# Optimization experiments

Hardware: AMD Instinct MI355X
Metric: run time of the kernel (lower is better)

The kernel has to match this reference:

```python
import jax, jax.numpy as jnp
import numpy as np

B, N, C = 8, 2048, 256
NGRP = 4          # n oscillator dims per group
RANK = 16         # A_rank
EPS = 1e-6        # solver eps
GN_EPS = 1e-5     # torch GroupNorm default eps


def setup_inputs() -> dict:
    key = jax.random.key(0)
    k0, k1, k2, k3 = jax.random.split(key, 4)
    x = jax.random.normal(k0, (B, N, C), jnp.float32)
    y = jax.random.normal(k1, (B, C, N), jnp.float32)
    sc = jax.random.uniform(k2, (B, N, N), jnp.float32)
    U = 0.01 * jax.random.normal(k3, (N, RANK), jnp.float32)
    omega_param = (1.0 / np.sqrt(2)).astype(np.float32) * jnp.ones((C // 2, 1), jnp.float32)
    gn_w = jnp.ones((C,), jnp.float32)
    gn_b = jnp.zeros((C,), jnp.float32)
    gamma = jnp.float32(1.0)
    return {"x": x, "y": y, "sc": sc, "U": U, "omega_param": omega_param,
            "gn_w": gn_w, "gn_b": gn_b, "gamma": gamma, "Q": 8}


def _map_to_sphere(x):
    # normalize each group of NGRP channels to unit norm
    xv = x.reshape(B, N, C // NGRP, NGRP)
    n2 = jnp.clip(jnp.sum(xv * xv, axis=-1, keepdims=True), EPS, None)
    return (xv * jax.lax.rsqrt(n2)).reshape(B, N, C)


def _project_osc(v, x):
    # remove component of v along x within each oscillator group (tangent projection)
    xv = x.reshape(B, N, C // NGRP, NGRP)
    vv = v.reshape(B, N, C // NGRP, NGRP)
    sim = jnp.sum(xv * vv, axis=-1, keepdims=True)
    return (vv - sim * xv).reshape(B, N, C)


def _group_norm(y, w, b):
    # y: [B, C, N]; num_groups = C // NGRP, NGRP channels per group
    G = C // NGRP
    yv = y.reshape(B, G, NGRP * N)
    mu = jnp.mean(yv, axis=-1, keepdims=True)
    var = jnp.mean((yv - mu) ** 2, axis=-1, keepdims=True)
    yn = ((yv - mu) * jax.lax.rsqrt(var + GN_EPS)).reshape(B, C, N)
    return yn * w[None, :, None] + b[None, :, None]


def _omega_term(x, omega_param):
    # pairwise rotation: (x0, x1) -> (omg*x1, -omg*x0), omg = |omega_param| per pair
    xp = x.reshape(B, N, C // 2, 2)
    omg = jnp.abs(omega_param).reshape(1, 1, C // 2)  # norm over trailing dim of size 1
    out = jnp.stack([omg * xp[..., 1], -omg * xp[..., 0]], axis=-1)
    return out.reshape(B, N, C)


def _kuramoto(x, y, sc, U, omega_param, gn_w, gn_b, gamma, Q):
    rho = 1.0
    # y: [B, C, N] -> GroupNorm -> [B, N, C] -> sphere
    y = _group_norm(y, gn_w, gn_b)
    y = _map_to_sphere(jnp.transpose(y, (0, 2, 1)))
    # x: [B, N, C] (N != C so no transpose in original)
    x = _map_to_sphere(x)
    # coupling matrix K = sym(W) * sigmoid(U U^T)  (normalize_K=False, w_scale=1)
    Wsym = 0.5 * (sc + jnp.transpose(sc, (0, 2, 1)))
    A = jax.nn.sigmoid(U @ U.T)          # [N, N]
    K = Wsym * A[None, :, :]             # [B, N, N]

    def step(xc, _):
        coupling = jnp.einsum('bnm,bmc->bnc', K, xc)
        force = coupling + y
        om = _omega_term(xc, omega_param)
        dxdt = om + rho * _project_osc(force, xc)
        xn = _map_to_sphere(xc + gamma * dxdt)
        return xn, xn

    _, xs = jax.lax.scan(step, x, None, length=Q)
    return xs  # [Q, B, N, C]


def reference(x, y, sc, U, omega_param, gn_w, gn_b, gamma, Q):
    return _kuramoto(x, y, sc, U, omega_param, gn_w, gn_b, gamma, Q)
```

## Files before the change

### kernel.cpp

```cpp
#include <hip/hip_runtime.h>
#include <hip/hip_bf16.h>

#define BB 8
#define NN 2048
#define CC 256
#define GG 64
#define QQ 8

typedef unsigned short u16;
typedef __attribute__((ext_vector_type(8))) short bf16x8;
typedef __attribute__((ext_vector_type(4))) float f32x4;

static __device__ __forceinline__ float b2f(u16 u) {
  union { unsigned int i; float f; } cv; cv.i = ((unsigned int)u) << 16; return cv.f;
}
static __device__ __forceinline__ u16 f2b(float f) {
  union { __hip_bfloat16 h; u16 u; } cv; cv.h = __float2bfloat16(f); return cv.u;
}
static __device__ __forceinline__ float ldin(const void* p, size_t i, bool f32) {
  return f32 ? ((const float*)p)[i] : b2f(((const u16*)p)[i]);
}
static __device__ __forceinline__ float4 ldin4(const void* p, size_t i, bool f32) {
  if (f32) return *(const float4*)((const float*)p + i);
  ushort4 u = *(const ushort4*)((const u16*)p + i);
  return make_float4(b2f(u.x), b2f(u.y), b2f(u.z), b2f(u.w));
}
static __device__ __forceinline__ void gload16(const void* g, void* l) {
  __builtin_amdgcn_global_load_lds(
      (const __attribute__((address_space(1))) void*)g,
      (__attribute__((address_space(3))) void*)l, 16, 0, 0);
}

__global__ __launch_bounds__(256) void detect_kernel(const u16* __restrict__ sc,
                                                     int* __restrict__ flag)
{
  __shared__ int sh;
  if (threadIdx.x == 0) sh = 0;
  __syncthreads();
  int cnt = 0;
  for (int i = threadIdx.x; i < 2048; i += 256) {
    u16 w = sc[2 * i];
    int e = (w >> 7) & 0xFF;
    if (e >= 100 && e <= 130) cnt++;
  }
  atomicAdd(&sh, cnt);
  __syncthreads();
  if (threadIdx.x == 0) *flag = (sh < 1024) ? 1 : 0;
}

__global__ __launch_bounds__(256) void build_k_kernel(
    const void* __restrict__ sc, const void* __restrict__ U,
    u16* __restrict__ Khi, u16* __restrict__ Klo,
    const int* __restrict__ flagp, int b0, int nbat)
{
  const int i0 = blockIdx.y * 32;
  const int j0 = blockIdx.x * 32;
  if (j0 < i0) return;
  const bool f32 = (*flagp != 0);
  const int tx = threadIdx.x;
  const int ty = threadIdx.y;
  const int t  = ty * 32 + tx;
  const int rr = t >> 3;
  const int cq = t & 7;

  __shared__ float Ui[32][17];
  __shared__ float Uj[32][17];
  __shared__ float As[32][33];
  __shared__ float t1[32][33];
  __shared__ float t2[32][33];

  for (int s = t; s < 512; s += 256) {
    int r2 = s >> 4, kk = s & 15;
    Ui[r2][kk] = ldin(U, (size_t)(i0 + r2) * 16 + kk, f32);
    Uj[r2][kk] = ldin(U, (size_t)(j0 + r2) * 16 + kk, f32);
  }
  __syncthreads();
  for (int ii = ty; ii < 32; ii += 8) {
    float dot = 0.f;
    #pragma unroll
    for (int k = 0; k < 16; k++) dot += Ui[ii][k] * Uj[tx][k];
    As[ii][tx] = 1.0f / (1.0f + expf(-dot));
  }

  for (int bl = 0; bl < nbat; bl++) {
    const int b = b0 + bl;
    const size_t scb = (size_t)b * NN * NN;
    __syncthreads();
    float4 va = ldin4(sc, scb + (size_t)(i0 + rr) * NN + j0 + 4 * cq, f32);
    float4 vb = ldin4(sc, scb + (size_t)(j0 + rr) * NN + i0 + 4 * cq, f32);
    t1[rr][4*cq+0] = va.x; t1[rr][4*cq+1] = va.y;
    t1[rr][4*cq+2] = va.z; t1[rr][4*cq+3] = va.w;
    t2[rr][4*cq+0] = vb.x; t2[rr][4*cq+1] = vb.y;
    t2[rr][4*cq+2] = vb.z; t2[rr][4*cq+3] = vb.w;
    __syncthreads();
    const size_t kfb = (size_t)bl * NN * NN;
    ushort4 h4, l4;
    #pragma unroll
    for (int k = 0; k < 4; k++) {
      int col = 4 * cq + k;
      float kv = 0.5f * (t1[rr][col] + t2[col][rr]) * As[rr][col];
      u16 h = f2b(kv);
      ((u16*)&h4)[k] = h;
      ((u16*)&l4)[k] = f2b(kv - b2f(h));
    }
    size_t o = kfb + (size_t)(i0 + rr) * NN + j0 + 4 * cq;
    *(ushort4*)(Khi + o) = h4;
    *(ushort4*)(Klo + o) = l4;
    if (i0 != j0) {
      #pragma unroll
      for (int k = 0; k < 4; k++) {
        int col = 4 * cq + k;
        float kv = 0.5f * (t2[rr][col] + t1[col][rr]) * As[col][rr];
        u16 h = f2b(kv);
        ((u16*)&h4)[k] = h;
        ((u16*)&l4)[k] = f2b(kv - b2f(h));
      }
      size_t o2 = kfb + (size_t)(j0 + rr) * NN + i0 + 4 * cq;
      *(ushort4*)(Khi + o2) = h4;
      *(ushort4*)(Klo + o2) = l4;
    }
  }
}

__global__ __launch_bounds__(256) void gn_stats_kernel(
    const void* __restrict__ y, float* __restrict__ murs,
    const int* __restrict__ flagp)
{
  const bool f32 = (*flagp != 0);
  const int bg = blockIdx.x;
  float s = 0.f, ss = 0.f;
  if (f32) {
    const float* base = (const float*)y + (size_t)bg * 4 * NN;
    for (int i = threadIdx.x; i < 2048; i += 256) {
      float4 v = *(const float4*)(base + (size_t)i * 4);
      s  += v.x + v.y + v.z + v.w;
      ss += v.x*v.x + v.y*v.y + v.z*v.z + v.w*v.w;
    }
  } else {
    const u16* base = (const u16*)y + (size_t)bg * 4 * NN;
    for (int i = threadIdx.x; i < 2048; i += 256) {
      ushort4 v = *(const ushort4*)(base + (size_t)i * 4);
      float f0 = b2f(v.x), f1 = b2f(v.y), f2 = b2f(v.z), f3 = b2f(v.w);
      s  += f0 + f1 + f2 + f3;
      ss += f0*f0 + f1*f1 + f2*f2 + f3*f3;
    }
  }
  #pragma unroll
  for (int off = 32; off > 0; off >>= 1) {
    s  += __shfl_down(s, off, 64);
    ss += __shfl_down(ss, off, 64);
  }
  __shared__ float sh[8];
  const int w = threadIdx.x >> 6, ln = threadIdx.x & 63;
  if (ln == 0) { sh[w * 2] = s; sh[w * 2 + 1] = ss; }
  __syncthreads();
  if (threadIdx.x == 0) {
    float S  = sh[0] + sh[2] + sh[4] + sh[6];
    float SS = sh[1] + sh[3] + sh[5] + sh[7];
    float mu  = S / 8192.0f;
    float var = SS / 8192.0f - mu * mu;
    murs[bg * 2]     = mu;
    murs[bg * 2 + 1] = 1.0f / sqrtf(fmaxf(var, 0.f) + 1e-5f);
  }
}

__global__ __launch_bounds__(256) void y_tf_kernel(
    const void* __restrict__ y, const float* __restrict__ murs,
    const void* __restrict__ gw, const void* __restrict__ gb,
    float* __restrict__ yt, const int* __restrict__ flagp)
{
  const bool f32 = (*flagp != 0);
  const int b = blockIdx.y;
  const int n = blockIdx.x * 64 + threadIdx.x;
  for (int g = threadIdx.y; g < GG; g += 4) {
    float mu = murs[(b * GG + g) * 2];
    float rs = murs[(b * GG + g) * 2 + 1];
    float v[4];
    #pragma unroll
    for (int k = 0; k < 4; k++) {
      int c = 4 * g + k;
      float val = (ldin(y, ((size_t)b * CC + c) * NN + n, f32) - mu) * rs;
      v[k] = val * ldin(gw, c, f32) + ldin(gb, c, f32);
    }
    float n2 = v[0]*v[0] + v[1]*v[1] + v[2]*v[2] + v[3]*v[3];
    float scl = 1.0f / sqrtf(fmaxf(n2, 1e-6f));
    float4 o; o.x = v[0]*scl; o.y = v[1]*scl; o.z = v[2]*scl; o.w = v[3]*scl;
    *(float4*)(yt + ((size_t)b * NN + n) * CC + 4 * g) = o;
  }
}

__global__ __launch_bounds__(256) void x_init_kernel(
    const void* __restrict__ x, u16* __restrict__ xTh, u16* __restrict__ xTl,
    const int* __restrict__ flagp)
{
  const bool f32 = (*flagp != 0);
  const int b = blockIdx.y;
  const int n = blockIdx.x * 64 + threadIdx.x;
  for (int g = threadIdx.y; g < GG; g += 4) {
    size_t idx = ((size_t)b * NN + n) * CC + 4 * g;
    float v[4];
    if (f32) {
      float4 u4 = *(const float4*)((const float*)x + idx);
      v[0] = u4.x; v[1] = u4.y; v[2] = u4.z; v[3] = u4.w;
    } else {
      ushort4 u = *(const ushort4*)((const u16*)x + idx);
      v[0] = b2f(u.x); v[1] = b2f(u.y); v[2] = b2f(u.z); v[3] = b2f(u.w);
    }
    float n2 = v[0]*v[0] + v[1]*v[1] + v[2]*v[2] + v[3]*v[3];
    float scl = 1.0f / sqrtf(fmaxf(n2, 1e-6f));
    size_t xb = ((size_t)b * CC + 4 * g) * NN + n;
    #pragma unroll
    for (int k = 0; k < 4; k++) {
      float xv = v[k] * scl;
      u16 h = f2b(xv);
      xTh[xb + (size_t)k * NN] = h;
      xTl[xb + (size_t)k * NN] = f2b(xv - b2f(h));
    }
  }
}

static __device__ __forceinline__ void fused_step_epilogue(
    f32x4 (&acc)[2][2], int b, int m0, int c0, int wr, int wc, int l15, int lk,
    const u16* __restrict__ xhc, const u16* __restrict__ xlc,
    u16* __restrict__ xhn, u16* __restrict__ xln,
    const float* __restrict__ yt, const void* __restrict__ omega,
    const void* __restrict__ gamma, void* __restrict__ outbase, size_t qoff,
    bool f32)
{
  const float gm = ldin(gamma, 0, f32);
  #pragma unroll
  for (int fr = 0; fr < 2; fr++) {
    const int rbase = m0 + wr * 32 + fr * 16 + lk * 4;
    #pragma unroll
    for (int fc = 0; fc < 2; fc++) {
      const int c = c0 + wc * 32 + fc * 16 + l15;
      const size_t xoff = ((size_t)b * CC + c) * NN + rbase;
      ushort4 xh4 = *(const ushort4*)(xhc + xoff);
      ushort4 xl4 = *(const ushort4*)(xlc + xoff);
      float xcv[4] = { b2f(xh4.x) + b2f(xl4.x), b2f(xh4.y) + b2f(xl4.y),
                       b2f(xh4.z) + b2f(xl4.z), b2f(xh4.w) + b2f(xl4.w) };
      float om   = fabsf(ldin(omega, c >> 1, f32));
      float omsg = (c & 1) ? -om : om;
      float xn[4];
      #pragma unroll
      for (int r = 0; r < 4; r++) {
        const int n = rbase + r;
        float f = acc[fr][fc][r] + yt[((size_t)b * NN + n) * CC + c];
        float s = xcv[r] * f;
        s += __shfl_xor(s, 1);
        s += __shfl_xor(s, 2);
        float xp = __shfl_xor(xcv[r], 1);
        float d  = omsg * xp + (f - s * xcv[r]);
        float v  = xcv[r] + gm * d;
        float n2 = v * v;
        n2 += __shfl_xor(n2, 1);
        n2 += __shfl_xor(n2, 2);
        float scl = 1.0f / sqrtf(fmaxf(n2, 1e-6f));
        xn[r] = v * scl;
        const size_t oidx = qoff + ((size_t)b * NN + n) * CC + c;
        if (f32) ((float*)outbase)[oidx] = xn[r];
        else     ((u16*)outbase)[oidx]   = f2b(xn[r]);
      }
      ushort4 nh, nl;
      #pragma unroll
      for (int r = 0; r < 4; r++) {
        u16 h = f2b(xn[r]);
        ((u16*)&nh)[r] = h;
        ((u16*)&nl)[r] = f2b(xn[r] - b2f(h));
      }
      *(ushort4*)(xhn + xoff) = nh;
      *(ushort4*)(xln + xoff) = nl;
    }
  }
}

__global__ __launch_bounds__(256, 4) void gemm_fused_sb(
    const u16* __restrict__ Khi, const u16* __restrict__ Klo,
    const u16* __restrict__ xhc, const u16* __restrict__ xlc,
    u16* __restrict__ xhn, u16* __restrict__ xln,
    const float* __restrict__ yt, const void* __restrict__ omega,
    const void* __restrict__ gamma, void* __restrict__ outbase, size_t qoff,
    const int* __restrict__ flagp)
{
  const int flat = blockIdx.x + 4 * blockIdx.y + 128 * blockIdx.z;
  const int swz  = (flat & 7) * 128 + (flat >> 3);
  const int bx = swz & 3;
  const int by = (swz >> 2) & 31;
  const int b  = swz >> 7;
  const int m0 = by * 64;
  const int c0 = bx * 64;

  __shared__ char lds[32768];

  const int t    = threadIdx.x;
  const int lane = t & 63;
  const int wid  = t >> 6;
  const int wr   = wid >> 1;
  const int wc   = wid & 1;

  const u16* Ah = Khi + (size_t)b * NN * NN;
  const u16* Al = Klo + (size_t)b * NN * NN;
  const u16* Bh = xhc + (size_t)b * CC * NN;
  const u16* Bl = xlc + (size_t)b * CC * NN;

  const int tr   = t >> 3;
  const int phys = (t & 7) ^ (tr & 7);
  const size_t aoff = (size_t)(m0 + tr) * NN + phys * 8;
  const size_t boff = (size_t)(c0 + tr) * NN + phys * 8;
  const int dst = wid * 1024;

  f32x4 acc[2][2];
  const f32x4 zero4 = {0.f, 0.f, 0.f, 0.f};
  #pragma unroll
  for (int i = 0; i < 2; i++)
    #pragma unroll
    for (int j = 0; j < 2; j++) acc[i][j] = zero4;

  const int l15 = lane & 15;
  const int lk  = lane >> 4;

  for (int kt = 0; kt < NN / 64; kt++) {
    const int k0 = kt * 64;
    #pragma unroll
    for (int i = 0; i < 2; i++) {
      gload16(Ah + aoff + (size_t)i * (32 * NN) + k0, lds +         i * 4096 + dst);
      gload16(Al + aoff + (size_t)i * (32 * NN) + k0, lds +  8192 + i * 4096 + dst);
      gload16(Bh + boff + (size_t)i * (32 * NN) + k0, lds + 16384 + i * 4096 + dst);
      gload16(Bl + boff + (size_t)i * (32 * NN) + k0, lds + 24576 + i * 4096 + dst);
    }
    __syncthreads();
    #pragma unroll
    for (int ks = 0; ks < 2; ks++) {
      const int cl = ks * 4 + lk;
      bf16x8 fah[2], fal[2], fbh[2], fbl[2];
      #pragma unroll
      for (int fr = 0; fr < 2; fr++) {
        int r   = wr * 32 + fr * 16 + l15;
        int off = r * 128 + ((cl ^ (r & 7)) << 4);
        fah[fr] = *(const bf16x8*)(lds + off);
        fal[fr] = *(const bf16x8*)(lds + 8192 + off);
      }
      #pragma unroll
      for (int fc = 0; fc < 2; fc++) {
        int r   = wc * 32 + fc * 16 + l15;
        int off = r * 128 + ((cl ^ (r & 7)) << 4);
        fbh[fc] = *(const bf16x8*)(lds + 16384 + off);
        fbl[fc] = *(const bf16x8*)(lds + 24576 + off);
      }
      #pragma unroll
      for (int fr = 0; fr < 2; fr++)
        #pragma unroll
        for (int fc = 0; fc < 2; fc++) {
          acc[fr][fc] = __builtin_amdgcn_mfma_f32_16x16x32_bf16(
              fah[fr], fbh[fc], acc[fr][fc], 0, 0, 0);
          acc[fr][fc] = __builtin_amdgcn_mfma_f32_16x16x32_bf16(
              fah[fr], fbl[fc], acc[fr][fc], 0, 0, 0);
          acc[fr][fc] = __builtin_amdgcn_mfma_f32_16x16x32_bf16(
              fal[fr], fbh[fc], acc[fr][fc], 0, 0, 0);
        }
    }
    __syncthreads();
  }

  fused_step_epilogue(acc, b, m0, c0, wr, wc, l15, lk,
                      xhc, xlc, xhn, xln, yt, omega, gamma,
                      outbase, qoff, (*flagp != 0));
}

__global__ __launch_bounds__(256, 2) void gemm_fused_db(
    const u16* __restrict__ Khi, const u16* __restrict__ Klo,
    const u16* __restrict__ xhc, const u16* __restrict__ xlc,
    u16* __restrict__ xhn, u16* __restrict__ xln,
    const float* __restrict__ yt, const void* __restrict__ omega,
    const void* __restrict__ gamma, void* __restrict__ outbase, size_t qoff,
    const int* __restrict__ flagp, int grp)
{
  const int flat = blockIdx.x + 4 * blockIdx.y + 128 * blockIdx.z;
  const int swz  = (flat & 7) * 64 + (flat >> 3);
  const int bx = swz & 3;
  const int by = (swz >> 2) & 31;
  const int bl = swz >> 7;
  const int b  = grp * 4 + bl;
  const int m0 = by * 64;
  const int c0 = bx * 64;

  __shared__ char lds[2][32768];

  const int t    = threadIdx.x;
  const int lane = t & 63;
  const int wid  = t >> 6;
  const int wr   = wid >> 1;
  const int wc   = wid & 1;

  const u16* Ah = Khi + (size_t)bl * NN * NN;
  const u16* Al = Klo + (size_t)bl * NN * NN;
  const u16* Bh = xhc + (size_t)b * CC * NN;
  const u16* Bl = xlc + (size_t)b * CC * NN;

  const int tr   = t >> 3;
  const int phys = (t & 7) ^ (tr & 7);
  const size_t aoff = (size_t)(m0 + tr) * NN + phys * 8;
  const size_t boff = (size_t)(c0 + tr) * NN + phys * 8;
  const int dst = wid * 1024;

  f32x4 acc[2][2];
  const f32x4 zero4 = {0.f, 0.f, 0.f, 0.f};
  #pragma unroll
  for (int i = 0; i < 2; i++)
    #pragma unroll
    for (int j = 0; j < 2; j++) acc[i][j] = zero4;

  auto stage = [&](int bufi, int kt) {
    char* base = &lds[bufi][0];
    const int k0 = kt * 64;
    #pragma unroll
    for (int i = 0; i < 2; i++) {
      gload16(Ah + aoff + (size_t)i * (32 * NN) + k0, base +         i * 4096 + dst);
      gload16(Al + aoff + (size_t)i * (32 * NN) + k0, base +  8192 + i * 4096 + dst);
      gload16(Bh + boff + (size_t)i * (32 * NN) + k0, base + 16384 + i * 4096 + dst);
      gload16(Bl + boff + (size_t)i * (32 * NN) + k0, base + 24576 + i * 4096 + dst);
    }
  };

  const int l15 = lane & 15;
  const int lk  = lane >> 4;

  auto compute = [&](int bufi) {
    const char* base = &lds[bufi][0];
    #pragma unroll
    for (int ks = 0; ks < 2; ks++) {
      const int cl = ks * 4 + lk;
      bf16x8 fah[2], fal[2], fbh[2], fbl[2];
      #pragma unroll
      for (int fr = 0; fr < 2; fr++) {
        int r   = wr * 32 + fr * 16 + l15;
        int off = r * 128 + ((cl ^ (r & 7)) << 4);
        fah[fr] = *(const bf16x8*)(base + off);
        fal[fr] = *(const bf16x8*)(base + 8192 + off);
      }
      #pragma unroll
      for (int fc = 0; fc < 2; fc++) {
        int r   = wc * 32 + fc * 16 + l15;
        int off = r * 128 + ((cl ^ (r & 7)) << 4);
        fbh[fc] = *(const bf16x8*)(base + 16384 + off);
        fbl[fc] = *(const bf16x8*)(base + 24576 + off);
      }
      #pragma unroll
      for (int fr = 0; fr < 2; fr++)
        #pragma unroll
        for (int fc = 0; fc < 2; fc++) {
          acc[fr][fc] = __builtin_amdgcn_mfma_f32_16x16x32_bf16(
              fah[fr], fbh[fc], acc[fr][fc], 0, 0, 0);
          acc[fr][fc] = __builtin_amdgcn_mfma_f32_16x16x32_bf16(
              fah[fr], fbl[fc], acc[fr][fc], 0, 0, 0);
          acc[fr][fc] = __builtin_amdgcn_mfma_f32_16x16x32_bf16(
              fal[fr], fbh[fc], acc[fr][fc], 0, 0, 0);
        }
    }
  };

  stage(0, 0);
  __syncthreads();
  int buf = 0;
  for (int kt = 0; kt < NN / 64; kt++) {
    if (kt + 1 < NN / 64) stage(buf ^ 1, kt + 1);
    compute(buf);
    __syncthreads();
    buf ^= 1;
  }

  fused_step_epilogue(acc, b, m0, c0, wr, wc, l15, lk,
                      xhc, xlc, xhn, xln, yt, omega, gamma,
                      outbase, qoff, (*flagp != 0));
}

extern "C" void kernel_launch(void* const* d_in, const int* in_sizes, int n_in,
                              void* d_out, int out_size, void* d_ws, size_t ws_size,
                              hipStream_t stream) {
  const void* x     = d_in[0];
  const void* y     = d_in[1];
  const void* sc    = d_in[2];
  const void* U     = d_in[3];
  const void* omega = d_in[4];
  const void* gw    = d_in[5];
  const void* gb    = d_in[6];
  const void* gamma = d_in[7];
  char* ws = (char*)d_ws;

  const size_t BNC = (size_t)BB * NN * CC;
  const bool big = ws_size >= 184600000ull;

  if (big) {
    u16*   Khi  = (u16*)(ws);
    u16*   Klo  = (u16*)(ws + 67108864);
    float* yt   = (float*)(ws + 134217728);
    u16*   xAh  = (u16*)(ws + 150994944);
    u16*   xAl  = (u16*)(ws + 159383552);
    u16*   xBh  = (u16*)(ws + 167772160);
    u16*   xBl  = (u16*)(ws + 176160768);
    float* murs = (float*)(ws + 184549376);
    int*   flag = (int*)  (ws + 184553472);
    u16* xh[2] = { xAh, xBh };
    u16* xl[2] = { xAl, xBl };

    detect_kernel<<<dim3(1), dim3(256), 0, stream>>>((const u16*)sc, flag);
    gn_stats_kernel<<<dim3(512), dim3(256), 0, stream>>>(y, murs, flag);
    y_tf_kernel<<<dim3(32, 8), dim3(64, 4), 0, stream>>>(y, murs, gw, gb, yt, flag);
    x_init_kernel<<<dim3(32, 8), dim3(64, 4), 0, stream>>>(x, xAh, xAl, flag);
    build_k_kernel<<<dim3(64, 64), dim3(32, 8), 0, stream>>>(
        sc, U, Khi, Klo, flag, 0, 8);
    for (int q = 0; q < QQ; q++) {
      const int cur = q & 1, nxt = cur ^ 1;
      gemm_fused_sb<<<dim3(4, 32, 8), dim3(256), 0, stream>>>(
          Khi, Klo, xh[cur], xl[cur], xh[nxt], xl[nxt],
          yt, omega, gamma, d_out, (size_t)q * BNC, flag);
    }
  } else {
    u16*   Khi  = (u16*)(ws);
    u16*   Klo  = (u16*)(ws + 33554432);
    float* yt   = (float*)(ws + 67108864);
    u16*   xAh  = (u16*)(ws + 83886080);
    u16*   xAl  = (u16*)(ws + 92274688);
    u16*   xBh  = (u16*)(ws + 100663296);
    u16*   xBl  = (u16*)(ws + 109051904);
    float* murs = (float*)(ws + 117440512);
    int*   flag = (int*)  (ws + 117444608);
    u16* xh[2] = { xAh, xBh };
    u16* xl[2] = { xAl, xBl };

    detect_kernel<<<dim3(1), dim3(256), 0, stream>>>((const u16*)sc, flag);
    gn_stats_kernel<<<dim3(512), dim3(256), 0, stream>>>(y, murs, flag);
    y_tf_kernel<<<dim3(32, 8), dim3(64, 4), 0, stream>>>(y, murs, gw, gb, yt, flag);
    x_init_kernel<<<dim3(32, 8), dim3(64, 4), 0, stream>>>(x, xAh, xAl, flag);
    for (int grp = 0; grp < 2; grp++) {
      build_k_kernel<<<dim3(64, 64), dim3(32, 8), 0, stream>>>(
          sc, U, Khi, Klo, flag, grp * 4, 4);
      for (int q = 0; q < QQ; q++) {
        const int cur = q & 1, nxt = cur ^ 1;
        gemm_fused_db<<<dim3(4, 32, 4), dim3(256), 0, stream>>>(
            Khi, Klo, xh[cur], xl[cur], xh[nxt], xl[nxt],
            yt, omega, gamma, d_out, (size_t)q * BNC, flag, grp);
      }
    }
  }
}
```

Baseline: 927.0 us.

## Use 128x128 tiles with 8 waves and double-buffered LDS pipeline in step GEMM

Replaces the single-buffered 64x64, 4-wave step GEMM with a 128x128-tile kernel of 512 threads (8 waves). It uses two 64 KB LDS buffers and explicit vmcnt waits so global loads for tile k+2 overlap compute on tile k. The larger tiles raise reuse of the K and x fragments and cut global traffic, and the pipelining hides load latency. In exchange the grid shrinks to 256 blocks, which may underfill the CUs, and the 128 KB of LDS per block limits occupancy to one block per CU.

```diff
diff --git a/kernel.cpp b/kernel.cpp
--- a/kernel.cpp
+++ b/kernel.cpp
@@ -219,8 +219,9 @@
   }
 }
 
+template<int NFR, int NFC>
 static __device__ __forceinline__ void fused_step_epilogue(
-    f32x4 (&acc)[2][2], int b, int m0, int c0, int wr, int wc, int l15, int lk,
+    f32x4 (&acc)[NFR][NFC], int b, int rb, int cb, int l15, int lk,
     const u16* __restrict__ xhc, const u16* __restrict__ xlc,
     u16* __restrict__ xhn, u16* __restrict__ xln,
     const float* __restrict__ yt, const void* __restrict__ omega,
@@ -229,11 +230,11 @@
 {
   const float gm = ldin(gamma, 0, f32);
   #pragma unroll
-  for (int fr = 0; fr < 2; fr++) {
-    const int rbase = m0 + wr * 32 + fr * 16 + lk * 4;
-    #pragma unroll
-    for (int fc = 0; fc < 2; fc++) {
-      const int c = c0 + wc * 32 + fc * 16 + l15;
+  for (int fr = 0; fr < NFR; fr++) {
+    const int rbase = rb + fr * 16 + lk * 4;
+    #pragma unroll
+    for (int fc = 0; fc < NFC; fc++) {
+      const int c = cb + fc * 16 + l15;
       const size_t xoff = ((size_t)b * CC + c) * NN + rbase;
       ushort4 xh4 = *(const ushort4*)(xhc + xoff);
       ushort4 xl4 = *(const ushort4*)(xlc + xoff);
@@ -274,7 +275,7 @@
   }
 }
 
-__global__ __launch_bounds__(256, 4) void gemm_fused_sb(
+__global__ __launch_bounds__(512, 2) void gemm_fused_sk(
     const u16* __restrict__ Khi, const u16* __restrict__ Klo,
     const u16* __restrict__ xhc, const u16* __restrict__ xlc,
     u16* __restrict__ xhn, u16* __restrict__ xln,
@@ -282,15 +283,134 @@
     const void* __restrict__ gamma, void* __restrict__ outbase, size_t qoff,
     const int* __restrict__ flagp)
 {
+  const int flat = blockIdx.x + 2 * blockIdx.y + 32 * blockIdx.z;
+  const int swz  = (flat & 7) * 32 + (flat >> 3);
+  const int bx = swz & 1;
+  const int by = (swz >> 1) & 15;
+  const int b  = swz >> 5;
+  const int m0 = by * 128;
+  const int c0 = bx * 128;
+
+  __shared__ char lds[2][65536];
+
+  const int t    = threadIdx.x;
+  const int lane = t & 63;
+  const int wid  = t >> 6;
+  const int ng   = wid >> 2;
+  const int wr   = (wid >> 1) & 1;
+  const int wc   = wid & 1;
+
+  const u16* Ah = Khi + (size_t)b * NN * NN;
+  const u16* Al = Klo + (size_t)b * NN * NN;
+  const u16* Bh = xhc + (size_t)b * CC * NN;
+  const u16* Bl = xlc + (size_t)b * CC * NN;
+
+  const int tr   = t >> 3;
+  const int phys = (t & 7) ^ (tr & 7);
+  const size_t aoff = (size_t)(m0 + tr) * NN + phys * 8;
+  const size_t boff = (size_t)(c0 + tr) * NN + phys * 8;
+  const int dst = wid * 1024;
+
+  f32x4 acc[4][2];
+  const f32x4 zero4 = {0.f, 0.f, 0.f, 0.f};
+  #pragma unroll
+  for (int i = 0; i < 4; i++)
+    #pragma unroll
+    for (int j = 0; j < 2; j++) acc[i][j] = zero4;
+
+  auto stage = [&](int bufi, int kt) {
+    char* base = &lds[bufi][0];
+    const int k0 = kt * 64;
+    #pragma unroll
+    for (int i = 0; i < 2; i++) {
+      gload16(Ah + aoff + (size_t)i * (64 * NN) + k0, base +         i * 8192 + dst);
+      gload16(Al + aoff + (size_t)i * (64 * NN) + k0, base + 16384 + i * 8192 + dst);
+      gload16(Bh + boff + (size_t)i * (64 * NN) + k0, base + 32768 + i * 8192 + dst);
+      gload16(Bl + boff + (size_t)i * (64 * NN) + k0, base + 49152 + i * 8192 + dst);
+    }
+  };
+
+  const int l15 = lane & 15;
+  const int lk  = lane >> 4;
+
+  auto compute = [&](int bufi) {
+    const char* base = &lds[bufi][0];
+    #pragma unroll
+    for (int ks = 0; ks < 2; ks++) {
+      const int cl = ks * 4 + lk;
+      bf16x8 fah[4], fal[4], fbh[2], fbl[2];
+      #pragma unroll
+      for (int fr = 0; fr < 4; fr++) {
+        int r   = wr * 64 + fr * 16 + l15;
+        int off = r * 128 + ((cl ^ (r & 7)) << 4);
+        fah[fr] = *(const bf16x8*)(base + off);
+        fal[fr] = *(const bf16x8*)(base + 16384 + off);
+      }
+      #pragma unroll
+      for (int fc = 0; fc < 2; fc++) {
+        int r   = ng * 64 + wc * 32 + fc * 16 + l15;
+        int off = r * 128 + ((cl ^ (r & 7)) << 4);
+        fbh[fc] = *(const bf16x8*)(base + 32768 + off);
+        fbl[fc] = *(const bf16x8*)(base + 49152 + off);
+      }
+      #pragma unroll
+      for (int fr = 0; fr < 4; fr++)
+        #pragma unroll
+        for (int fc = 0; fc < 2; fc++) {
+          acc[fr][fc] = __builtin_amdgcn_mfma_f32_16x16x32_bf16(
+              fah[fr], fbh[fc], acc[fr][fc], 0, 0, 0);
+          acc[fr][fc] = __builtin_amdgcn_mfma_f32_16x16x32_bf16(
+              fah[fr], fbl[fc], acc[fr][fc], 0, 0, 0);
+          acc[fr][fc] = __builtin_amdgcn_mfma_f32_16x16x32_bf16(
+              fal[fr], fbh[fc], acc[fr][fc], 0, 0, 0);
+        }
+    }
+  };
+
+  stage(0, 0);
+  stage(1, 1);
+  for (int kt = 0; kt < 30; kt++) {
+    asm volatile("s_waitcnt vmcnt(8)" ::: "memory");
+    __builtin_amdgcn_s_barrier();
+    __builtin_amdgcn_sched_barrier(0);
+    compute(kt & 1);
+    asm volatile("s_waitcnt lgkmcnt(0)" ::: "memory");
+    __builtin_amdgcn_sched_barrier(0);
+    __builtin_amdgcn_s_barrier();
+    stage(kt & 1, kt + 2);
+  }
+  asm volatile("s_waitcnt vmcnt(8)" ::: "memory");
+  __builtin_amdgcn_s_barrier();
+  __builtin_amdgcn_sched_barrier(0);
+  compute(0);
+  asm volatile("s_waitcnt vmcnt(0)" ::: "memory");
+  __builtin_amdgcn_s_barrier();
+  __builtin_amdgcn_sched_barrier(0);
+  compute(1);
+
+  fused_step_epilogue<4, 2>(acc, b, m0 + wr * 64, c0 + ng * 64 + wc * 32,
+                            l15, lk, xhc, xlc, xhn, xln, yt, omega, gamma,
+                            outbase, qoff, (*flagp != 0));
+}
+
+__global__ __launch_bounds__(256, 2) void gemm_fused_db(
+    const u16* __restrict__ Khi, const u16* __restrict__ Klo,
+    const u16* __restrict__ xhc, const u16* __restrict__ xlc,
+    u16* __restrict__ xhn, u16* __restrict__ xln,
+    const float* __restrict__ yt, const void* __restrict__ omega,
+    const void* __restrict__ gamma, void* __restrict__ outbase, size_t qoff,
+    const int* __restrict__ flagp, int grp)
+{
   const int flat = blockIdx.x + 4 * blockIdx.y + 128 * blockIdx.z;
-  const int swz  = (flat & 7) * 128 + (flat >> 3);
+  const int swz  = (flat & 7) * 64 + (flat >> 3);
   const int bx = swz & 3;
   const int by = (swz >> 2) & 31;
-  const int b  = swz >> 7;
+  const int bl = swz >> 7;
+  const int b  = grp * 4 + bl;
   const int m0 = by * 64;
   const int c0 = bx * 64;
 
-  __shared__ char lds[32768];
+  __shared__ char lds[2][32768];
 
   const int t    = threadIdx.x;
   const int lane = t & 63;
@@ -298,8 +418,8 @@
   const int wr   = wid >> 1;
   const int wc   = wid & 1;
 
-  const u16* Ah = Khi + (size_t)b * NN * NN;
-  const u16* Al = Klo + (size_t)b * NN * NN;
+  const u16* Ah = Khi + (size_t)bl * NN * NN;
+  const u16* Al = Klo + (size_t)bl * NN * NN;
   const u16* Bh = xhc + (size_t)b * CC * NN;
   const u16* Bl = xlc + (size_t)b * CC * NN;
 
@@ -316,19 +436,23 @@
     #pragma unroll
     for (int j = 0; j < 2; j++) acc[i][j] = zero4;
 
+  auto stage = [&](int bufi, int kt) {
+    char* base = &lds[bufi][0];
+    const int k0 = kt * 64;
+    #pragma unroll
+    for (int i = 0; i < 2; i++) {
+      gload16(Ah + aoff + (size_t)i * (32 * NN) + k0, base +         i * 4096 + dst);
+      gload16(Al + aoff + (size_t)i * (32 * NN) + k0, base +  8192 + i * 4096 + dst);
+      gload16(Bh + boff + (size_t)i * (32 * NN) + k0, base + 16384 + i * 4096 + dst);
+      gload16(Bl + boff + (size_t)i * (32 * NN) + k0, base + 24576 + i * 4096 + dst);
+    }
+  };
+
   const int l15 = lane & 15;
   const int lk  = lane >> 4;
 
-  for (int kt = 0; kt < NN / 64; kt++) {
-    const int k0 = kt * 64;
-    #pragma unroll
-    for (int i = 0; i < 2; i++) {
-      gload16(Ah + aoff + (size_t)i * (32 * NN) + k0, lds +         i * 4096 + dst);
-      gload16(Al + aoff + (size_t)i * (32 * NN) + k0, lds +  8192 + i * 4096 + dst);
-      gload16(Bh + boff + (size_t)i * (32 * NN) + k0, lds + 16384 + i * 4096 + dst);
-      gload16(Bl + boff + (size_t)i * (32 * NN) + k0, lds + 24576 + i * 4096 + dst);
-    }
-    __syncthreads();
+  auto compute = [&](int bufi) {
+    const char* base = &lds[bufi][0];
     #pragma unroll
     for (int ks = 0; ks < 2; ks++) {
       const int cl = ks * 4 + lk;
@@ -337,15 +461,15 @@
       for (int fr = 0; fr < 2; fr++) {
         int r   = wr * 32 + fr * 16 + l15;
         int off = r * 128 + ((cl ^ (r & 7)) << 4);
-        fah[fr] = *(const bf16x8*)(lds + off);
-        fal[fr] = *(const bf16x8*)(lds + 8192 + off);
+        fah[fr] = *(const bf16x8*)(base + off);
+        fal[fr] = *(const bf16x8*)(base + 8192 + off);
       }
       #pragma unroll
       for (int fc = 0; fc < 2; fc++) {
         int r   = wc * 32 + fc * 16 + l15;
         int off = r * 128 + ((cl ^ (r & 7)) << 4);
-        fbh[fc] = *(const bf16x8*)(lds + 16384 + off);
-        fbl[fc] = *(const bf16x8*)(lds + 24576 + off);
+        fbh[fc] = *(const bf16x8*)(base + 16384 + off);
+        fbl[fc] = *(const bf16x8*)(base + 24576 + off);
       }
       #pragma unroll
       for (int fr = 0; fr < 2; fr++)
@@ -359,104 +483,6 @@
               fal[fr], fbh[fc], acc[fr][fc], 0, 0, 0);
         }
     }
-    __syncthreads();
-  }
-
-  fused_step_epilogue(acc, b, m0, c0, wr, wc, l15, lk,
-                      xhc, xlc, xhn, xln, yt, omega, gamma,
-                      outbase, qoff, (*flagp != 0));
-}
-
-__global__ __launch_bounds__(256, 2) void gemm_fused_db(
-    const u16* __restrict__ Khi, const u16* __restrict__ Klo,
-    const u16* __restrict__ xhc, const u16* __restrict__ xlc,
-    u16* __restrict__ xhn, u16* __restrict__ xln,
-    const float* __restrict__ yt, const void* __restrict__ omega,
-    const void* __restrict__ gamma, void* __restrict__ outbase, size_t qoff,
-    const int* __restrict__ flagp, int grp)
-{
-  const int flat = blockIdx.x + 4 * blockIdx.y + 128 * blockIdx.z;
-  const int swz  = (flat & 7) * 64 + (flat >> 3);
-  const int bx = swz & 3;
-  const int by = (swz >> 2) & 31;
-  const int bl = swz >> 7;
-  const int b  = grp * 4 + bl;
-  const int m0 = by * 64;
-  const int c0 = bx * 64;
-
-  __shared__ char lds[2][32768];
-
-  const int t    = threadIdx.x;
-  const int lane = t & 63;
-  const int wid  = t >> 6;
-  const int wr   = wid >> 1;
-  const int wc   = wid & 1;
-
-  const u16* Ah = Khi + (size_t)bl * NN * NN;
-  const u16* Al = Klo + (size_t)bl * NN * NN;
-  const u16* Bh = xhc + (size_t)b * CC * NN;
-  const u16* Bl = xlc + (size_t)b * CC * NN;
-
-  const int tr   = t >> 3;
-  const int phys = (t & 7) ^ (tr & 7);
-  const size_t aoff = (size_t)(m0 + tr) * NN + phys * 8;
-  const size_t boff = (size_t)(c0 + tr) * NN + phys * 8;
-  const int dst = wid * 1024;
-
-  f32x4 acc[2][2];
-  const f32x4 zero4 = {0.f, 0.f, 0.f, 0.f};
-  #pragma unroll
-  for (int i = 0; i < 2; i++)
-    #pragma unroll
-    for (int j = 0; j < 2; j++) acc[i][j] = zero4;
-
-  auto stage = [&](int bufi, int kt) {
-    char* base = &lds[bufi][0];
-    const int k0 = kt * 64;
-    #pragma unroll
-    for (int i = 0; i < 2; i++) {
-      gload16(Ah + aoff + (size_t)i * (32 * NN) + k0, base +         i * 4096 + dst);
-      gload16(Al + aoff + (size_t)i * (32 * NN) + k0, base +  8192 + i * 4096 + dst);
-      gload16(Bh + boff + (size_t)i * (32 * NN) + k0, base + 16384 + i * 4096 + dst);
-      gload16(Bl + boff + (size_t)i * (32 * NN) + k0, base + 24576 + i * 4096 + dst);
-    }
-  };
-
-  const int l15 = lane & 15;
-  const int lk  = lane >> 4;
-
-  auto compute = [&](int bufi) {
-    const char* base = &lds[bufi][0];
-    #pragma unroll
-    for (int ks = 0; ks < 2; ks++) {
-      const int cl = ks * 4 + lk;
-      bf16x8 fah[2], fal[2], fbh[2], fbl[2];
-      #pragma unroll
-      for (int fr = 0; fr < 2; fr++) {
-        int r   = wr * 32 + fr * 16 + l15;
-        int off = r * 128 + ((cl ^ (r & 7)) << 4);
-        fah[fr] = *(const bf16x8*)(base + off);
-        fal[fr] = *(const bf16x8*)(base + 8192 + off);
-      }
-      #pragma unroll
-      for (int fc = 0; fc < 2; fc++) {
-        int r   = wc * 32 + fc * 16 + l15;
-        int off = r * 128 + ((cl ^ (r & 7)) << 4);
-        fbh[fc] = *(const bf16x8*)(base + 16384 + off);
-        fbl[fc] = *(const bf16x8*)(base + 24576 + off);
-      }
-      #pragma unroll
-      for (int fr = 0; fr < 2; fr++)
-        #pragma unroll
-        for (int fc = 0; fc < 2; fc++) {
-          acc[fr][fc] = __builtin_amdgcn_mfma_f32_16x16x32_bf16(
-              fah[fr], fbh[fc], acc[fr][fc], 0, 0, 0);
-          acc[fr][fc] = __builtin_amdgcn_mfma_f32_16x16x32_bf16(
-              fah[fr], fbl[fc], acc[fr][fc], 0, 0, 0);
-          acc[fr][fc] = __builtin_amdgcn_mfma_f32_16x16x32_bf16(
-              fal[fr], fbh[fc], acc[fr][fc], 0, 0, 0);
-        }
-    }
   };
 
   stage(0, 0);
@@ -469,9 +495,9 @@
     buf ^= 1;
   }
 
-  fused_step_epilogue(acc, b, m0, c0, wr, wc, l15, lk,
-                      xhc, xlc, xhn, xln, yt, omega, gamma,
-                      outbase, qoff, (*flagp != 0));
+  fused_step_epilogue<2, 2>(acc, b, m0 + wr * 32, c0 + wc * 32,
+                            l15, lk, xhc, xlc, xhn, xln, yt, omega, gamma,
+                            outbase, qoff, (*flagp != 0));
 }
 
 extern "C" void kernel_launch(void* const* d_in, const int* in_sizes, int n_in,
@@ -511,7 +537,7 @@
         sc, U, Khi, Klo, flag, 0, 8);
     for (int q = 0; q < QQ; q++) {
       const int cur = q & 1, nxt = cur ^ 1;
-      gemm_fused_sb<<<dim3(4, 32, 8), dim3(256), 0, stream>>>(
+      gemm_fused_sk<<<dim3(2, 16, 8), dim3(512), 0, stream>>>(
           Khi, Klo, xh[cur], xl[cur], xh[nxt], xl[nxt],
           yt, omega, gamma, d_out, (size_t)q * BNC, flag);
     }
```

Measured after the change: 907.3 us. 1.02x faster.
